# Performance work log

Hardware: AMD Instinct MI355X
Metric: run time of the kernel (lower is better)

The kernel has to match this reference:

```python
import jax, jax.numpy as jnp
import numpy as np

EPS = 1e-6  # F.pairwise_distance default eps, added to the difference


def setup_inputs() -> dict:
    key = jax.random.key(0)
    k1, k2 = jax.random.split(key)
    N, NS, NQ, D = 2048, 5, 8, 256
    x = jax.random.normal(k1, (N, NS + NQ, D), dtype=jnp.float32)
    label = jax.random.randint(k2, (N,), 0, N, dtype=jnp.int64)
    return {"x": x, "label": label, "n_s": NS, "n_q": NQ}


def reference(x, label, n_s, n_q):
    # x: [N, n_s+n_q, D]
    anchors = jnp.mean(x[:, :n_s, :], axis=1)               # [N, D] prototypes
    N, D = anchors.shape
    queries = x[:, n_s:n_s + n_q, :].reshape(N * n_q, D)     # [N*n_q, D]

    # Exact ||q - a + eps||^2 via GEMM expansion (matches F.pairwise_distance(.,.)**2):
    # ||q-a||^2 + 2*eps*sum(q-a) + D*eps^2
    q_sq = jnp.sum(queries * queries, axis=-1)               # [N*n_q]
    a_sq = jnp.sum(anchors * anchors, axis=-1)               # [N]
    cross = queries @ anchors.T                              # [N*n_q, N]
    q_sum = jnp.sum(queries, axis=-1)                        # [N*n_q]
    a_sum = jnp.sum(anchors, axis=-1)                        # [N]
    dist_sq = (q_sq[:, None] + a_sq[None, :] - 2.0 * cross
               + 2.0 * EPS * (q_sum[:, None] - a_sum[None, :])
               + D * EPS * EPS)
    logits = -dist_sq                                        # [N*n_q, N]

    lab = jnp.repeat(label, n_q)                             # [N*n_q]
    logp = jax.nn.log_softmax(logits, axis=-1)
    nloss = -jnp.mean(jnp.take_along_axis(logp, lab[:, None], axis=1))
    prec1 = jnp.mean((jnp.argmax(logits, axis=-1) == lab).astype(jnp.float32)) * 100.0
    return nloss, prec1
```

## Files before the change

kernel.cpp:

```cpp
#include <hip/hip_runtime.h>
#include <math.h>

#define EPS  1e-6f
#define DD   256
#define NSUP 5
#define NQ   8
#define SEQ  13
#define L2E  1.44269504088896f
#define LN2  0.693147180559945f
#define NEP  2048
#define NROW 16384
#define NCOL 2048

typedef short bf16x8 __attribute__((ext_vector_type(8)));
typedef float f32x4  __attribute__((ext_vector_type(4)));

__device__ __forceinline__ ushort f2bf(float f) {
  union { float f; unsigned u; } v; v.f = f;
  unsigned r = v.u + 0x7FFFu + ((v.u >> 16) & 1u);
  return (ushort)(r >> 16);
}

__global__ __launch_bounds__(256) void proto_prep(
    const float* __restrict__ x, float* __restrict__ cb,
    ushort* __restrict__ Asw, ushort* __restrict__ Qsw,
    float* __restrict__ accum, int* __restrict__ counter) {
  const int n = blockIdx.x, d = threadIdx.x;
  if (n == 0 && d == 0) { accum[0] = 0.f; accum[1] = 0.f; counter[0] = 0; }
  const float* xr = x + (size_t)n * SEQ * DD;

  const int kk = d >> 5, quad = (d >> 3) & 3, j = d & 7;
  const size_t dpart = (size_t)kk * 64 + quad * 16;

  float a = 0.f;
  #pragma unroll
  for (int s = 0; s < NSUP; ++s) a += xr[s * DD + d];
  a *= 0.2f;
  Asw[(((size_t)(n >> 4) * 8 * 64) + dpart + (n & 15)) * 8 + j] = f2bf(a);

  float s1 = a, s2 = a * a;
  #pragma unroll
  for (int off = 32; off; off >>= 1) {
    s1 += __shfl_xor(s1, off);
    s2 += __shfl_xor(s2, off);
  }
  __shared__ float red[8];
  const int wid = d >> 6, lane = d & 63;
  if (lane == 0) { red[wid] = s1; red[wid + 4] = s2; }
  __syncthreads();
  if (d == 0) {
    float t1 = red[0] + red[1] + red[2] + red[3];
    float t2 = red[4] + red[5] + red[6] + red[7];
    cb[n] = -L2E * (t2 - 2.f * EPS * t1);
  }
  #pragma unroll
  for (int s = 0; s < NQ; ++s) {
    const int row = n * NQ + s;
    Qsw[(((size_t)(row >> 4) * 8 * 64) + dpart + (row & 15)) * 8 + j]
        = f2bf(xr[(NSUP + s) * DD + d]);
  }
}

__global__ __launch_bounds__(256, 2) void proto_main(
    const ushort* __restrict__ Qsw, const ushort* __restrict__ Asw,
    const float* __restrict__ cb, const int* __restrict__ label,
    float* __restrict__ accum, int* __restrict__ counter,
    float* __restrict__ out) {
  const int tid  = threadIdx.x;
  const int wid  = tid >> 6, lane = tid & 63;
  const int quad = lane >> 4, lcol = lane & 15;
  const int r0   = blockIdx.x * 32;

  const bf16x8* qb = (const bf16x8*)Qsw;
  const bf16x8* bb = (const bf16x8*)Asw;

  bf16x8 af[2][8];
  #pragma unroll
  for (int set = 0; set < 2; ++set) {
    const size_t base = ((size_t)((r0 >> 4) + set) * 8) * 64 + lane;
    #pragma unroll
    for (int kk = 0; kk < 8; ++kk) af[set][kk] = qb[base + (size_t)kk * 64];
  }

  float m[2][4], s[2][4], ll[2][4];
  int   bi[2][4], lab[2][4];
  #pragma unroll
  for (int set = 0; set < 2; ++set)
    #pragma unroll
    for (int i = 0; i < 4; ++i) {
      m[set][i] = -1e30f; s[set][i] = 0.f; ll[set][i] = 0.f;
      bi[set][i] = 0x7fffffff;
      lab[set][i] = label[(r0 + set * 16 + quad * 4 + i) >> 3];
    }

  auto process = [&](int T, bf16x8* B) {
    f32x4 c0 = {0.f, 0.f, 0.f, 0.f}, c1 = {0.f, 0.f, 0.f, 0.f};
    #pragma unroll
    for (int kk = 0; kk < 8; ++kk) {
      c0 = __builtin_amdgcn_mfma_f32_16x16x32_bf16(af[0][kk], B[kk], c0, 0, 0, 0);
      c1 = __builtin_amdgcn_mfma_f32_16x16x32_bf16(af[1][kk], B[kk], c1, 0, 0, 0);
    }
    const int   colIdx = T * 16 + lcol;
    const float cbv    = cb[colIdx];
    #pragma unroll
    for (int set = 0; set < 2; ++set) {
      #pragma unroll
      for (int i = 0; i < 4; ++i) {
        float cv = (set == 0) ? c0[i] : c1[i];
        float v2 = fmaf(cv, 2.f * L2E, cbv);
        float dv = v2 - m[set][i];
        bool  gt = dv > 0.f;
        float e  = exp2f(-fabsf(dv));
        s[set][i]  = fmaf(s[set][i], gt ? e : 1.f, gt ? 1.f : e);
        m[set][i]  = gt ? v2 : m[set][i];
        bi[set][i] = gt ? colIdx : bi[set][i];
        ll[set][i] = (colIdx == lab[set][i]) ? v2 : ll[set][i];
      }
    }
  };

  const int T0 = wid * 32;
  bf16x8 buf0[8], buf1[8];
  #pragma unroll
  for (int kk = 0; kk < 8; ++kk)
    buf0[kk] = bb[((size_t)T0 * 8 + (size_t)kk) * 64 + lane];

  #pragma unroll 1
  for (int t = 0; t < 32; t += 2) {
    {
      const int Tn = T0 + t + 1;
      #pragma unroll
      for (int kk = 0; kk < 8; ++kk)
        buf1[kk] = bb[((size_t)Tn * 8 + (size_t)kk) * 64 + lane];
    }
    process(T0 + t, buf0);
    {
      const int Tn = (t + 2 < 32) ? T0 + t + 2 : T0 + t + 1;
      #pragma unroll
      for (int kk = 0; kk < 8; ++kk)
        buf0[kk] = bb[((size_t)Tn * 8 + (size_t)kk) * 64 + lane];
    }
    process(T0 + t + 1, buf1);
  }

  #pragma unroll
  for (int mask = 1; mask < 16; mask <<= 1) {
    #pragma unroll
    for (int set = 0; set < 2; ++set)
      #pragma unroll
      for (int i = 0; i < 4; ++i) {
        float om = __shfl_xor(m[set][i], mask);
        float os = __shfl_xor(s[set][i], mask);
        int   oi = __shfl_xor(bi[set][i], mask);
        float ol = __shfl_xor(ll[set][i], mask);
        float nm = fmaxf(m[set][i], om);
        s[set][i] = s[set][i] * exp2f(m[set][i] - nm) + os * exp2f(om - nm);
        bool better = (om > m[set][i]) || (om == m[set][i] && oi < bi[set][i]);
        bi[set][i] = better ? oi : bi[set][i];
        m[set][i]  = nm;
        ll[set][i] += ol;
      }
  }

  __shared__ float sm[4][32], ssh[4][32], sll[4][32];
  __shared__ int   sbi[4][32];
  if (lcol == 0) {
    #pragma unroll
    for (int set = 0; set < 2; ++set)
      #pragma unroll
      for (int i = 0; i < 4; ++i) {
        int rl = set * 16 + quad * 4 + i;
        sm[wid][rl] = m[set][i];  ssh[wid][rl] = s[set][i];
        sll[wid][rl] = ll[set][i]; sbi[wid][rl] = bi[set][i];
      }
  }
  __syncthreads();
  if (tid < 32) {
    float mm = sm[0][tid], sv = ssh[0][tid], lv = sll[0][tid];
    int   b  = sbi[0][tid];
    #pragma unroll
    for (int w = 1; w < 4; ++w) {
      float om = sm[w][tid], os = ssh[w][tid];
      int   oi = sbi[w][tid];
      float nm = fmaxf(mm, om);
      sv = sv * exp2f(mm - nm) + os * exp2f(om - nm);
      bool better = (om > mm) || (om == mm && oi < b);
      b = better ? oi : b;
      mm = nm;
      lv += sll[w][tid];
    }
    const int row = r0 + tid;
    const int lb  = label[row >> 3];
    float loss = LN2 * (mm + log2f(sv) - lv);
    float corr = (b == lb) ? 1.f : 0.f;
    #pragma unroll
    for (int mask = 16; mask; mask >>= 1) {
      loss += __shfl_xor(loss, mask);
      corr += __shfl_xor(corr, mask);
    }
    if (tid == 0) {
      atomicAdd(&accum[0], loss);
      atomicAdd(&accum[1], corr);
      __threadfence();
      if (atomicAdd(counter, 1) == (int)gridDim.x - 1) {
        out[0] = atomicAdd(&accum[0], 0.f) / (float)NROW;
        out[1] = atomicAdd(&accum[1], 0.f) * 100.f / (float)NROW;
      }
    }
  }
}

extern "C" void kernel_launch(void* const* d_in, const int* in_sizes, int n_in,
                              void* d_out, int out_size, void* d_ws, size_t ws_size,
                              hipStream_t stream) {
  const float* x     = (const float*)d_in[0];
  const int*   label = (const int*)d_in[1];
  float* out = (float*)d_out;

  float*  W       = (float*)d_ws;
  float*  accum   = W;
  int*    counter = (int*)(W + 2);
  float*  cb      = W + 16;
  ushort* Asw     = (ushort*)(cb + NCOL);
  ushort* Qsw     = Asw + (size_t)NCOL * DD;

  hipLaunchKernelGGL(proto_prep, dim3(NEP), dim3(256), 0, stream,
                     x, cb, Asw, Qsw, accum, counter);
  hipLaunchKernelGGL(proto_main, dim3(NROW / 32), dim3(256), 0, stream,
                     Qsw, Asw, cb, label, accum, counter, out);
}
```

Measured before the change: 124.5 us.

## Split columns across eight waves and compute label logit with a direct dot

Doubles the block to 512 threads so each of eight waves handles 16 column tiles instead of 32, which shortens the per-wave serial loop and raises occupancy. The per-element label-logit tracking is removed from the inner online-softmax loop. The target logit is instead recomputed once per row with a small bf16 dot product between the query and its labelled prototype, reduced across 16 lanes. This trims registers and VALU work in the hot loop, at the cost of a larger cross-wave shared-memory reduction and some extra gather loads.

```diff
diff --git a/kernel.cpp b/kernel.cpp
--- a/kernel.cpp
+++ b/kernel.cpp
@@ -20,6 +20,10 @@
   unsigned r = v.u + 0x7FFFu + ((v.u >> 16) & 1u);
   return (ushort)(r >> 16);
 }
+__device__ __forceinline__ float bf2f(short u) {
+  union { unsigned u; float f; } v; v.u = ((unsigned)(unsigned short)u) << 16;
+  return v.f;
+}
 
 __global__ __launch_bounds__(256) void proto_prep(
     const float* __restrict__ x, float* __restrict__ cb,
@@ -61,7 +65,7 @@
   }
 }
 
-__global__ __launch_bounds__(256, 2) void proto_main(
+__global__ __launch_bounds__(512, 4) void proto_main(
     const ushort* __restrict__ Qsw, const ushort* __restrict__ Asw,
     const float* __restrict__ cb, const int* __restrict__ label,
     float* __restrict__ accum, int* __restrict__ counter,
@@ -82,15 +86,13 @@
     for (int kk = 0; kk < 8; ++kk) af[set][kk] = qb[base + (size_t)kk * 64];
   }
 
-  float m[2][4], s[2][4], ll[2][4];
-  int   bi[2][4], lab[2][4];
+  float m[2][4], s[2][4];
+  int   bi[2][4];
   #pragma unroll
   for (int set = 0; set < 2; ++set)
     #pragma unroll
     for (int i = 0; i < 4; ++i) {
-      m[set][i] = -1e30f; s[set][i] = 0.f; ll[set][i] = 0.f;
-      bi[set][i] = 0x7fffffff;
-      lab[set][i] = label[(r0 + set * 16 + quad * 4 + i) >> 3];
+      m[set][i] = -1e30f; s[set][i] = 0.f; bi[set][i] = 0x7fffffff;
     }
 
   auto process = [&](int T, bf16x8* B) {
@@ -112,21 +114,20 @@
         bool  gt = dv > 0.f;
         float e  = exp2f(-fabsf(dv));
         s[set][i]  = fmaf(s[set][i], gt ? e : 1.f, gt ? 1.f : e);
-        m[set][i]  = gt ? v2 : m[set][i];
+        m[set][i]  = fmaxf(m[set][i], v2);
         bi[set][i] = gt ? colIdx : bi[set][i];
-        ll[set][i] = (colIdx == lab[set][i]) ? v2 : ll[set][i];
       }
     }
   };
 
-  const int T0 = wid * 32;
+  const int T0 = wid * 16;
   bf16x8 buf0[8], buf1[8];
   #pragma unroll
   for (int kk = 0; kk < 8; ++kk)
     buf0[kk] = bb[((size_t)T0 * 8 + (size_t)kk) * 64 + lane];
 
   #pragma unroll 1
-  for (int t = 0; t < 32; t += 2) {
+  for (int t = 0; t < 16; t += 2) {
     {
       const int Tn = T0 + t + 1;
       #pragma unroll
@@ -135,7 +136,7 @@
     }
     process(T0 + t, buf0);
     {
-      const int Tn = (t + 2 < 32) ? T0 + t + 2 : T0 + t + 1;
+      const int Tn = (t + 2 < 16) ? T0 + t + 2 : T0 + t + 1;
       #pragma unroll
       for (int kk = 0; kk < 8; ++kk)
         buf0[kk] = bb[((size_t)Tn * 8 + (size_t)kk) * 64 + lane];
@@ -152,34 +153,53 @@
         float om = __shfl_xor(m[set][i], mask);
         float os = __shfl_xor(s[set][i], mask);
         int   oi = __shfl_xor(bi[set][i], mask);
-        float ol = __shfl_xor(ll[set][i], mask);
         float nm = fmaxf(m[set][i], om);
         s[set][i] = s[set][i] * exp2f(m[set][i] - nm) + os * exp2f(om - nm);
         bool better = (om > m[set][i]) || (om == m[set][i] && oi < bi[set][i]);
         bi[set][i] = better ? oi : bi[set][i];
         m[set][i]  = nm;
-        ll[set][i] += ol;
-      }
-  }
-
-  __shared__ float sm[4][32], ssh[4][32], sll[4][32];
-  __shared__ int   sbi[4][32];
+      }
+  }
+
+  __shared__ float sm[8][32], ssh[8][32], slab[32];
+  __shared__ int   sbi[8][32];
   if (lcol == 0) {
     #pragma unroll
     for (int set = 0; set < 2; ++set)
       #pragma unroll
       for (int i = 0; i < 4; ++i) {
         int rl = set * 16 + quad * 4 + i;
-        sm[wid][rl] = m[set][i];  ssh[wid][rl] = s[set][i];
-        sll[wid][rl] = ll[set][i]; sbi[wid][rl] = bi[set][i];
-      }
+        sm[wid][rl] = m[set][i]; ssh[wid][rl] = s[set][i]; sbi[wid][rl] = bi[set][i];
+      }
+  }
+
+  {
+    const int g = tid >> 4, l = tid & 15;
+    const int row = r0 + g;
+    const int lab = label[row >> 3];
+    const size_t qc = ((size_t)(row >> 4) * 8 + (l >> 1)) * 64
+                    + (size_t)((2 * l) & 3) * 16 + (row & 15);
+    const size_t ac = ((size_t)(lab >> 4) * 8 + (l >> 1)) * 64
+                    + (size_t)((2 * l) & 3) * 16 + (lab & 15);
+    bf16x8 q0 = qb[qc], q1 = qb[qc + 16];
+    bf16x8 a0 = bb[ac], a1 = bb[ac + 16];
+    float dot = 0.f;
+    #pragma unroll
+    for (int j = 0; j < 8; ++j) {
+      dot = fmaf(bf2f(q0[j]), bf2f(a0[j]), dot);
+      dot = fmaf(bf2f(q1[j]), bf2f(a1[j]), dot);
+    }
+    #pragma unroll
+    for (int mask = 1; mask < 16; mask <<= 1) dot += __shfl_xor(dot, mask);
+    if (l == 0) slab[g] = fmaf(dot, 2.f * L2E, cb[lab]);
   }
   __syncthreads();
+
   if (tid < 32) {
-    float mm = sm[0][tid], sv = ssh[0][tid], lv = sll[0][tid];
+    float mm = sm[0][tid], sv = ssh[0][tid];
     int   b  = sbi[0][tid];
     #pragma unroll
-    for (int w = 1; w < 4; ++w) {
+    for (int w = 1; w < 8; ++w) {
       float om = sm[w][tid], os = ssh[w][tid];
       int   oi = sbi[w][tid];
       float nm = fmaxf(mm, om);
@@ -187,11 +207,10 @@
       bool better = (om > mm) || (om == mm && oi < b);
       b = better ? oi : b;
       mm = nm;
-      lv += sll[w][tid];
     }
     const int row = r0 + tid;
     const int lb  = label[row >> 3];
-    float loss = LN2 * (mm + log2f(sv) - lv);
+    float loss = LN2 * (mm + log2f(sv) - slab[tid]);
     float corr = (b == lb) ? 1.f : 0.f;
     #pragma unroll
     for (int mask = 16; mask; mask >>= 1) {
@@ -226,6 +245,6 @@
 
   hipLaunchKernelGGL(proto_prep, dim3(NEP), dim3(256), 0, stream,
                      x, cb, Asw, Qsw, accum, counter);
-  hipLaunchKernelGGL(proto_main, dim3(NROW / 32), dim3(256), 0, stream,
+  hipLaunchKernelGGL(proto_main, dim3(NROW / 32), dim3(512), 0, stream,
                      Qsw, Asw, cb, label, accum, counter, out);
 }
```

After: 156.1 us. 1.25x slower.
